# Optimization experiments

Measured on AMD Instinct MI355X. Metric: run time of the kernel, lower is better.

## Reference

```python
import jax, jax.numpy as jnp
import numpy as np

D_MODEL, D_STATE, D_CONV, EXPAND = 1024, 16, 4, 2
D_INNER = D_MODEL * EXPAND
BATCH, SEQ = 2, 2048


def setup_inputs() -> dict:
    key = jax.random.key(0)
    ks = jax.random.split(key, 10)
    s = lambda *sh: 1.0 / np.sqrt(sh[-1])
    x = jax.random.normal(ks[0], (BATCH, SEQ, D_MODEL), jnp.float32)
    W_in = jax.random.normal(ks[1], (2 * D_INNER, D_MODEL), jnp.float32) * s(D_MODEL)
    conv_w = jax.random.normal(ks[2], (D_INNER, 1, D_CONV), jnp.float32) * s(D_CONV)
    conv_b = jax.random.normal(ks[3], (D_INNER,), jnp.float32) * 0.01
    W_x = jax.random.normal(ks[4], (2 * D_STATE + 1, D_INNER), jnp.float32) * s(D_INNER)
    W_dt = jax.random.normal(ks[5], (D_INNER, 1), jnp.float32)
    b_dt = jax.random.normal(ks[6], (D_INNER,), jnp.float32) * 0.01
    A_log = jnp.log(jnp.broadcast_to(jnp.arange(1, D_STATE + 1, dtype=jnp.float32), (D_INNER, D_STATE)))
    D = jnp.ones((D_INNER,), jnp.float32)
    W_out = jax.random.normal(ks[7], (D_MODEL, D_INNER), jnp.float32) * s(D_INNER)
    return {"x": x, "W_in": W_in, "conv_w": conv_w, "conv_b": conv_b,
            "W_x": W_x, "W_dt": W_dt, "b_dt": b_dt, "A_log": A_log, "D": D, "W_out": W_out}


def _selective_ssm(x, W_in, conv_w, conv_b, W_x, W_dt, b_dt, A_log, D, W_out):
    B_, L, _ = x.shape
    d_inner = conv_w.shape[0]
    d_conv = conv_w.shape[-1]
    d_state = A_log.shape[-1]
    # input projection -> (x, z), each [B, L, d_inner]
    xz = jnp.einsum('bld,ed->ble', x, W_in)
    xi, z = jnp.split(xz, 2, axis=-1)
    # depthwise causal conv over time (torch pads both sides then slices [:L] == left-pad)
    x_ncl = jnp.moveaxis(xi, 1, 2)  # [B, d_inner, L]
    x_conv = jax.lax.conv_general_dilated(
        x_ncl, conv_w, window_strides=(1,), padding=[(d_conv - 1, 0)],
        dimension_numbers=('NCH', 'OIH', 'NCH'), feature_group_count=d_inner)
    x_conv = x_conv + conv_b[None, :, None]
    xi = jax.nn.silu(jnp.moveaxis(x_conv, 1, 2))  # [B, L, d_inner]
    # selective parameters
    x_dbl = jnp.einsum('bld,ed->ble', xi, W_x)  # [B, L, 2*d_state+1]
    dt_raw = x_dbl[..., :1]
    Bmat = x_dbl[..., 1:1 + d_state]
    Cmat = x_dbl[..., 1 + d_state:]
    dt = jax.nn.softplus(dt_raw * W_dt[None, None, :, 0] + b_dt)  # [B, L, d_inner]
    A = -jnp.exp(A_log)  # [d_inner, d_state]
    # recurrence: h_t = exp(dt_t*A)*h_{t-1} + (dt_t*B_t)*x_t ; y_t = <h_t, C_t>
    def step(h, inp):
        x_t, dt_t, B_t, C_t = inp  # [B,d], [B,d], [B,n], [B,n]
        dA = jnp.exp(dt_t[..., None] * A)              # [B, d, n]
        dB = dt_t[..., None] * B_t[:, None, :]          # [B, d, n]
        h = dA * h + dB * x_t[..., None]
        y = jnp.einsum('bdn,bn->bd', h, C_t)
        return h, y

    h0 = jnp.zeros((B_, d_inner, d_state), xi.dtype)
    xs = (jnp.moveaxis(xi, 0, 1), jnp.moveaxis(dt, 0, 1),
          jnp.moveaxis(Bmat, 0, 1), jnp.moveaxis(Cmat, 0, 1))
    _, ys = jax.lax.scan(step, h0, xs)                 # [L, B, d_inner]
    y = jnp.moveaxis(ys, 0, 1) + D * xi                # skip term D*x_t
    y = y * jax.nn.silu(z)
    return jnp.einsum('bld,ed->ble', y, W_out)


def reference(x, W_in, conv_w, conv_b, W_x, W_dt, b_dt, A_log, D, W_out):
    return _selective_ssm(x, W_in, conv_w, conv_b, W_x, W_dt, b_dt, A_log, D, W_out)
```

## Files before the change

### kernel.cpp

```cpp
#include <hip/hip_runtime.h>
#include <hip/hip_bf16.h>

#define D_MODEL 1024
#define D_STATE 16
#define D_CONV  4
#define D_INNER 2048
#define BATCH   2
#define SEQ     2048
#define NTOK    (BATCH * SEQ)
#define NXZ     (2 * D_INNER)
#define NDBL    (2 * D_STATE + 1)
#define XROW    40
#define CHUNK   32
#define NCHUNK  (SEQ / CHUNK)
#define XT      4

typedef __attribute__((ext_vector_type(8))) short bf16x8;
typedef __attribute__((ext_vector_type(4))) float f32x4;

__device__ __forceinline__ float silu_fast(float x) {
    return x / (1.0f + __expf(-x));
}
__device__ __forceinline__ float softplus_fast(float x) {
    float r = __logf(1.0f + __expf(x));
    return (x > 20.f) ? x : r;
}
__device__ __forceinline__ short f2bf(float f) {
    __hip_bfloat16 h = __float2bfloat16(f);
    return __builtin_bit_cast(short, h);
}
__device__ __forceinline__ float bf2f(short s) {
    return __bfloat162float(__builtin_bit_cast(__hip_bfloat16, s));
}
__device__ __forceinline__ void gload_lds16(const void* g, void* l) {
    __builtin_amdgcn_global_load_lds(
        (const __attribute__((address_space(1))) void*)g,
        (__attribute__((address_space(3))) void*)l, 16, 0, 0);
}

__global__ void split_kernel(const float* __restrict__ in, short* __restrict__ hi,
                             short* __restrict__ lo, int n4)
{
    int i = blockIdx.x * blockDim.x + threadIdx.x;
    if (i >= n4) return;
    float4 v = ((const float4*)in)[i];
    short4 h, l;
    h.x = f2bf(v.x); l.x = f2bf(v.x - bf2f(h.x));
    h.y = f2bf(v.y); l.y = f2bf(v.y - bf2f(h.y));
    h.z = f2bf(v.z); l.z = f2bf(v.z - bf2f(h.z));
    h.w = f2bf(v.w); l.w = f2bf(v.w - bf2f(h.w));
    ((short4*)hi)[i] = h;
    ((short4*)lo)[i] = l;
}

__launch_bounds__(256, 3)
__global__ void mfma_gemm_split(const short* __restrict__ Ahi, const short* __restrict__ Alo,
                                const short* __restrict__ Bhi, const short* __restrict__ Blo,
                                float* __restrict__ C, int M, int N, int K)
{
    __shared__ short sAh[4096], sAl[4096], sBh[4096], sBl[4096];
    const int tid  = threadIdx.x;
    const int lane = tid & 63;
    const int wave = tid >> 6;
    const int bm = blockIdx.y, bn = blockIdx.x;
    const int wm = wave >> 1, wn = wave & 1;

    const int r0a = bm * 128, r0b = bn * 128;

    auto stage = [&](int k0) {
#pragma unroll
        for (int i = 0; i < 2; ++i) {
            const int off = i * 4096 + tid * 16;
            const int g   = off >> 11;
            const int row = (off >> 4) & 127;
            const size_t ea = (size_t)(r0a + row) * K + k0 + g * 8;
            const size_t eb = (size_t)(r0b + row) * K + k0 + g * 8;
            gload_lds16(Ahi + ea, (char*)sAh + i * 4096 + wave * 1024);
            gload_lds16(Alo + ea, (char*)sAl + i * 4096 + wave * 1024);
            gload_lds16(Bhi + eb, (char*)sBh + i * 4096 + wave * 1024);
            gload_lds16(Blo + eb, (char*)sBl + i * 4096 + wave * 1024);
        }
    };

    f32x4 acc[4][4] = {};

    stage(0);
    for (int k0 = 0; k0 < K; k0 += 32) {
        __syncthreads();

        const int g = lane >> 4;
        bf16x8 ah[4], al[4], bh[4], bl[4];
#pragma unroll
        for (int m = 0; m < 4; ++m) {
            const int rowA = wm * 64 + m * 16 + (lane & 15);
            const int rowB = wn * 64 + m * 16 + (lane & 15);
            ah[m] = ((const bf16x8*)sAh)[g * 128 + rowA];
            al[m] = ((const bf16x8*)sAl)[g * 128 + rowA];
            bh[m] = ((const bf16x8*)sBh)[g * 128 + rowB];
            bl[m] = ((const bf16x8*)sBl)[g * 128 + rowB];
        }
        __syncthreads();

        if (k0 + 32 < K) stage(k0 + 32);

#pragma unroll
        for (int m = 0; m < 4; ++m)
#pragma unroll
            for (int n = 0; n < 4; ++n) {
                acc[m][n] = __builtin_amdgcn_mfma_f32_16x16x32_bf16(ah[m], bh[n], acc[m][n], 0, 0, 0);
                acc[m][n] = __builtin_amdgcn_mfma_f32_16x16x32_bf16(ah[m], bl[n], acc[m][n], 0, 0, 0);
                acc[m][n] = __builtin_amdgcn_mfma_f32_16x16x32_bf16(al[m], bh[n], acc[m][n], 0, 0, 0);
            }
    }

#pragma unroll
    for (int m = 0; m < 4; ++m) {
        const int row = bm * 128 + wm * 64 + m * 16 + ((lane >> 4) << 2);
#pragma unroll
        for (int n = 0; n < 4; ++n) {
            const int col = bn * 128 + wn * 64 + n * 16 + (lane & 15);
#pragma unroll
            for (int r = 0; r < 4; ++r)
                C[(size_t)(row + r) * N + col] = acc[m][n][r];
        }
    }
}

__global__ void conv_silu_kernel(const float* __restrict__ xz,
                                 const float* __restrict__ conv_w,
                                 const float* __restrict__ conv_b,
                                 float* __restrict__ xi)
{
    int idx = blockIdx.x * blockDim.x + threadIdx.x;
    if (idx >= NTOK * D_INNER) return;
    int d = idx % D_INNER;
    int t = idx / D_INNER;
    int l = t % SEQ;
    int b = t / SEQ;

    float w0 = conv_w[d * 4 + 0], w1 = conv_w[d * 4 + 1];
    float w2 = conv_w[d * 4 + 2], w3 = conv_w[d * 4 + 3];

    const float* base = xz + ((size_t)b * SEQ) * NXZ + d;
    float acc = conv_b[d];
    if (l >= 3) acc = fmaf(w0, base[(size_t)(l - 3) * NXZ], acc);
    if (l >= 2) acc = fmaf(w1, base[(size_t)(l - 2) * NXZ], acc);
    if (l >= 1) acc = fmaf(w2, base[(size_t)(l - 1) * NXZ], acc);
    acc = fmaf(w3, base[(size_t)l * NXZ], acc);
    xi[idx] = silu_fast(acc);
}

__launch_bounds__(256)
__global__ void xdbl_kernel(const float* __restrict__ xi,
                            const float* __restrict__ W_x,
                            float* __restrict__ xdbl)
{
    __shared__ float rows[XT][D_INNER];
    const int t0 = blockIdx.x * XT;
    for (int i = threadIdx.x; i < XT * D_INNER; i += 256)
        rows[i >> 11][i & 2047] = xi[(size_t)(t0 + (i >> 11)) * D_INNER + (i & 2047)];
    __syncthreads();

    const int wave = threadIdx.x >> 6;
    const int lane = threadIdx.x & 63;
    for (int e = wave; e < NDBL; e += 4) {
        const float* wr = W_x + (size_t)e * D_INNER;
        float s0 = 0.f, s1 = 0.f, s2 = 0.f, s3 = 0.f;
        for (int i = lane; i < D_INNER; i += 64) {
            float w = wr[i];
            s0 = fmaf(rows[0][i], w, s0);
            s1 = fmaf(rows[1][i], w, s1);
            s2 = fmaf(rows[2][i], w, s2);
            s3 = fmaf(rows[3][i], w, s3);
        }
#pragma unroll
        for (int off = 32; off; off >>= 1) {
            s0 += __shfl_xor(s0, off);
            s1 += __shfl_xor(s1, off);
            s2 += __shfl_xor(s2, off);
            s3 += __shfl_xor(s3, off);
        }
        if (lane == 0) {
            const int slot = (e == 0 ? 0 : e + 3);
            xdbl[(size_t)(t0 + 0) * XROW + slot] = s0;
            xdbl[(size_t)(t0 + 1) * XROW + slot] = s1;
            xdbl[(size_t)(t0 + 2) * XROW + slot] = s2;
            xdbl[(size_t)(t0 + 3) * XROW + slot] = s3;
        }
    }
}

__launch_bounds__(256)
__global__ void scan_pass1(const float* __restrict__ xdbl,
                           const float* __restrict__ xi,
                           const float* __restrict__ W_dt,
                           const float* __restrict__ b_dt,
                           const float* __restrict__ A_log,
                           float* __restrict__ aprod,
                           float* __restrict__ hloc)
{
    const int d = blockIdx.x * 256 + threadIdx.x;
    const int c = blockIdx.y;
    const int b = blockIdx.z;

    float A[16];
    {
        const float4* ar = (const float4*)(A_log + (size_t)d * 16);
#pragma unroll
        for (int q = 0; q < 4; ++q) {
            float4 v = ar[q];
            A[q * 4 + 0] = -__expf(v.x);
            A[q * 4 + 1] = -__expf(v.y);
            A[q * 4 + 2] = -__expf(v.z);
            A[q * 4 + 3] = -__expf(v.w);
        }
    }
    const float wdt = W_dt[d], bdt = b_dt[d];

    const float* xd = xdbl + ((size_t)b * SEQ + c * CHUNK) * XROW;
    const float* xp = xi + ((size_t)b * SEQ + c * CHUNK) * D_INNER + d;

    float h[16], ap[16], Bv[16];
#pragma unroll
    for (int n = 0; n < 16; ++n) { h[n] = 0.f; ap[n] = 1.f; }

    for (int l = 0; l < CHUNK; ++l) {
        float raw = xd[0];
#pragma unroll
        for (int q = 0; q < 4; ++q) {
            float4 v = *(const float4*)(xd + 4 + q * 4);
            Bv[q * 4 + 0] = v.x; Bv[q * 4 + 1] = v.y;
            Bv[q * 4 + 2] = v.z; Bv[q * 4 + 3] = v.w;
        }
        float xv = xp[0];
        float dtv = softplus_fast(fmaf(raw, wdt, bdt));
        float dtx = dtv * xv;
#pragma unroll
        for (int n = 0; n < 16; ++n) {
            float e = __expf(dtv * A[n]);
            h[n]  = fmaf(e, h[n], Bv[n] * dtx);
            ap[n] *= e;
        }
        xd += XROW; xp += D_INNER;
    }

    size_t s = (((size_t)b * NCHUNK + c) * D_INNER + d) * 16;
#pragma unroll
    for (int q = 0; q < 4; ++q) {
        *(float4*)(aprod + s + q * 4) = make_float4(ap[q*4], ap[q*4+1], ap[q*4+2], ap[q*4+3]);
        *(float4*)(hloc  + s + q * 4) = make_float4(h[q*4],  h[q*4+1],  h[q*4+2],  h[q*4+3]);
    }
}

__global__ void scan_combine(float* __restrict__ aprod,
                             const float* __restrict__ hloc)
{
    int idx = blockIdx.x * blockDim.x + threadIdx.x;
    int b  = idx >> 15;
    int dn = idx & 32767;
    float hs = 0.f;
#pragma unroll
    for (int c = 0; c < NCHUNK; ++c) {
        size_t s = (((size_t)b * NCHUNK + c) << 15) + dn;
        float ap = aprod[s];
        float hl = hloc[s];
        aprod[s] = hs;
        hs = fmaf(ap, hs, hl);
    }
}

__launch_bounds__(256)
__global__ void scan_pass2(const float* __restrict__ xdbl,
                           float* __restrict__ xi,
                           const float* __restrict__ xz,
                           const float* __restrict__ W_dt,
                           const float* __restrict__ b_dt,
                           const float* __restrict__ A_log,
                           const float* __restrict__ Dvec,
                           const float* __restrict__ hstart)
{
    const int d = blockIdx.x * 256 + threadIdx.x;
    const int c = blockIdx.y;
    const int b = blockIdx.z;

    float A[16];
    {
        const float4* ar = (const float4*)(A_log + (size_t)d * 16);
#pragma unroll
        for (int q = 0; q < 4; ++q) {
            float4 v = ar[q];
            A[q * 4 + 0] = -__expf(v.x);
            A[q * 4 + 1] = -__expf(v.y);
            A[q * 4 + 2] = -__expf(v.z);
            A[q * 4 + 3] = -__expf(v.w);
        }
    }
    const float wdt = W_dt[d], bdt = b_dt[d], Dd = Dvec[d];

    const float* xd = xdbl + ((size_t)b * SEQ + c * CHUNK) * XROW;
    float*       xp = xi + ((size_t)b * SEQ + c * CHUNK) * D_INNER + d;
    const float* zp = xz + ((size_t)b * SEQ + c * CHUNK) * NXZ + D_INNER + d;

    float h[16], Bv[16], Cv[16];
    {
        size_t s = (((size_t)b * NCHUNK + c) * D_INNER + d) * 16;
#pragma unroll
        for (int q = 0; q < 4; ++q) {
            float4 v = *(const float4*)(hstart + s + q * 4);
            h[q * 4 + 0] = v.x; h[q * 4 + 1] = v.y;
            h[q * 4 + 2] = v.z; h[q * 4 + 3] = v.w;
        }
    }

    for (int l = 0; l < CHUNK; ++l) {
        float raw = xd[0];
#pragma unroll
        for (int q = 0; q < 4; ++q) {
            float4 v = *(const float4*)(xd + 4 + q * 4);
            Bv[q * 4 + 0] = v.x; Bv[q * 4 + 1] = v.y;
            Bv[q * 4 + 2] = v.z; Bv[q * 4 + 3] = v.w;
            float4 w = *(const float4*)(xd + 20 + q * 4);
            Cv[q * 4 + 0] = w.x; Cv[q * 4 + 1] = w.y;
            Cv[q * 4 + 2] = w.z; Cv[q * 4 + 3] = w.w;
        }
        float xv = xp[0];
        float zv = zp[0];
        float dtv = softplus_fast(fmaf(raw, wdt, bdt));
        float dtx = dtv * xv;

        float p0 = 0.f, p1 = 0.f, p2 = 0.f, p3 = 0.f;
#pragma unroll
        for (int q = 0; q < 4; ++q) {
            float e0 = __expf(dtv * A[q*4+0]);
            float e1 = __expf(dtv * A[q*4+1]);
            float e2 = __expf(dtv * A[q*4+2]);
            float e3 = __expf(dtv * A[q*4+3]);
            h[q*4+0] = fmaf(e0, h[q*4+0], Bv[q*4+0] * dtx);
            h[q*4+1] = fmaf(e1, h[q*4+1], Bv[q*4+1] * dtx);
            h[q*4+2] = fmaf(e2, h[q*4+2], Bv[q*4+2] * dtx);
            h[q*4+3] = fmaf(e3, h[q*4+3], Bv[q*4+3] * dtx);
            p0 = fmaf(h[q*4+0], Cv[q*4+0], p0);
            p1 = fmaf(h[q*4+1], Cv[q*4+1], p1);
            p2 = fmaf(h[q*4+2], Cv[q*4+2], p2);
            p3 = fmaf(h[q*4+3], Cv[q*4+3], p3);
        }
        float y = (p0 + p1) + (p2 + p3) + Dd * xv;
        xp[0] = y * silu_fast(zv);

        xd += XROW; xp += D_INNER; zp += NXZ;
    }
}

extern "C" void kernel_launch(void* const* d_in, const int* in_sizes, int n_in,
                              void* d_out, int out_size, void* d_ws, size_t ws_size,
                              hipStream_t stream)
{
    (void)in_sizes; (void)n_in; (void)out_size; (void)ws_size;

    const float* x      = (const float*)d_in[0];
    const float* W_in   = (const float*)d_in[1];
    const float* conv_w = (const float*)d_in[2];
    const float* conv_b = (const float*)d_in[3];
    const float* W_x    = (const float*)d_in[4];
    const float* W_dt   = (const float*)d_in[5];
    const float* b_dt   = (const float*)d_in[6];
    const float* A_log  = (const float*)d_in[7];
    const float* Dvec   = (const float*)d_in[8];
    const float* W_out  = (const float*)d_in[9];
    float* out = (float*)d_out;

    float* xz   = (float*)d_ws;
    float* xi   = xz + (size_t)NTOK * NXZ;
    float* xdbl = xi + (size_t)NTOK * D_INNER;
    float* R    = xdbl + (size_t)NTOK * XROW;

    short* x_hi   = (short*)R;
    short* x_lo   = x_hi + (size_t)NTOK * D_MODEL;
    short* Win_hi = x_lo + (size_t)NTOK * D_MODEL;
    short* Win_lo = Win_hi + (size_t)NXZ * D_MODEL;
    float* aprod  = R;
    float* hloc   = aprod + (size_t)BATCH * NCHUNK * D_INNER * 16;
    short* y_hi   = (short*)xz;
    short* y_lo   = y_hi + (size_t)NTOK * D_INNER;
    short* Wou_hi = y_lo + (size_t)NTOK * D_INNER;
    short* Wou_lo = Wou_hi + (size_t)D_MODEL * D_INNER;

    split_kernel<<<(NTOK * D_MODEL / 4 + 255) / 256, 256, 0, stream>>>(x, x_hi, x_lo, NTOK * D_MODEL / 4);
    split_kernel<<<(NXZ * D_MODEL / 4 + 255) / 256, 256, 0, stream>>>(W_in, Win_hi, Win_lo, NXZ * D_MODEL / 4);

    {
        dim3 grid(NXZ / 128, NTOK / 128);
        mfma_gemm_split<<<grid, 256, 0, stream>>>(x_hi, x_lo, Win_hi, Win_lo, xz, NTOK, NXZ, D_MODEL);
    }
    {
        int total = NTOK * D_INNER;
        conv_silu_kernel<<<(total + 255) / 256, 256, 0, stream>>>(xz, conv_w, conv_b, xi);
    }
    xdbl_kernel<<<NTOK / XT, 256, 0, stream>>>(xi, W_x, xdbl);

    {
        dim3 grid(D_INNER / 256, NCHUNK, BATCH);
        scan_pass1<<<grid, 256, 0, stream>>>(xdbl, xi, W_dt, b_dt, A_log, aprod, hloc);
        scan_combine<<<(BATCH * D_INNER * 16) / 256, 256, 0, stream>>>(aprod, hloc);
        scan_pass2<<<grid, 256, 0, stream>>>(xdbl, xi, xz, W_dt, b_dt, A_log, Dvec, aprod);
    }
    split_kernel<<<(NTOK * D_INNER / 4 + 255) / 256, 256, 0, stream>>>(xi, y_hi, y_lo, NTOK * D_INNER / 4);
    split_kernel<<<(D_MODEL * D_INNER / 4 + 255) / 256, 256, 0, stream>>>(W_out, Wou_hi, Wou_lo, D_MODEL * D_INNER / 4);
    {
        dim3 grid(D_MODEL / 128, NTOK / 128);
        mfma_gemm_split<<<grid, 256, 0, stream>>>(y_hi, y_lo, Wou_hi, Wou_lo, out, NTOK, D_MODEL, D_INNER);
    }
}
```

Measured before the change: 595.7 us.

## Double-buffer LDS in split GEMM, add split-K and XCD-aware block remap

The split-bf16 MFMA GEMM now uses two LDS buffers, so the next K-tile load is issued before computing the current one and one barrier per step is dropped. Workgroup IDs are remapped in groups of 8, apparently to spread adjacent tiles across XCDs. The output projection becomes a 2-way split-K, writing partial results into the free xi buffer, followed by an add kernel. This trades double the LDS (lower occupancy bound) and extra partial-sum traffic for better latency hiding and more workgroups on the small-N GEMM.

```diff
diff --git a/kernel.cpp b/kernel.cpp
--- a/kernel.cpp
+++ b/kernel.cpp
@@ -53,21 +53,33 @@
     ((short4*)lo)[i] = l;
 }
 
-__launch_bounds__(256, 3)
+__launch_bounds__(256, 2)
 __global__ void mfma_gemm_split(const short* __restrict__ Ahi, const short* __restrict__ Alo,
                                 const short* __restrict__ Bhi, const short* __restrict__ Blo,
-                                float* __restrict__ C, int M, int N, int K)
-{
-    __shared__ short sAh[4096], sAl[4096], sBh[4096], sBl[4096];
+                                float* __restrict__ C, int M, int N, int K,
+                                int kLen, size_t partStride)
+{
+    __shared__ short sAh[2][4096], sAl[2][4096], sBh[2][4096], sBl[2][4096];
     const int tid  = threadIdx.x;
     const int lane = tid & 63;
     const int wave = tid >> 6;
-    const int bm = blockIdx.y, bn = blockIdx.x;
     const int wm = wave >> 1, wn = wave & 1;
 
+    const int gx = gridDim.x, gy = gridDim.y;
+    const int nwg = gx * gy * gridDim.z;
+    int f = (blockIdx.z * gy + blockIdx.y) * gx + blockIdx.x;
+    f = (f & 7) * (nwg >> 3) + (f >> 3);
+    const int bz  = f / (gx * gy);
+    const int rem = f % (gx * gy);
+    const int bm = rem / gx;
+    const int bn = rem % gx;
+
+    const int kBeg = bz * kLen;
+    float* Cp = C + (size_t)bz * partStride;
+
     const int r0a = bm * 128, r0b = bn * 128;
 
-    auto stage = [&](int k0) {
+    auto stage = [&](int k0, int buf) {
 #pragma unroll
         for (int i = 0; i < 2; ++i) {
             const int off = i * 4096 + tid * 16;
@@ -75,34 +87,39 @@
             const int row = (off >> 4) & 127;
             const size_t ea = (size_t)(r0a + row) * K + k0 + g * 8;
             const size_t eb = (size_t)(r0b + row) * K + k0 + g * 8;
-            gload_lds16(Ahi + ea, (char*)sAh + i * 4096 + wave * 1024);
-            gload_lds16(Alo + ea, (char*)sAl + i * 4096 + wave * 1024);
-            gload_lds16(Bhi + eb, (char*)sBh + i * 4096 + wave * 1024);
-            gload_lds16(Blo + eb, (char*)sBl + i * 4096 + wave * 1024);
+            const int dst = buf * 8192 + i * 4096 + wave * 1024;
+            gload_lds16(Ahi + ea, (char*)sAh + dst);
+            gload_lds16(Alo + ea, (char*)sAl + dst);
+            gload_lds16(Bhi + eb, (char*)sBh + dst);
+            gload_lds16(Blo + eb, (char*)sBl + dst);
         }
     };
 
     f32x4 acc[4][4] = {};
-
-    stage(0);
-    for (int k0 = 0; k0 < K; k0 += 32) {
+    const int nsteps = kLen / 32;
+
+    stage(kBeg, 0);
+    for (int s = 0; s < nsteps; ++s) {
         __syncthreads();
-
+        if (s + 1 < nsteps) stage(kBeg + (s + 1) * 32, (s + 1) & 1);
+
+        const int buf = s & 1;
         const int g = lane >> 4;
+        const bf16x8* pAh = (const bf16x8*)sAh + buf * 512 + g * 128;
+        const bf16x8* pAl = (const bf16x8*)sAl + buf * 512 + g * 128;
+        const bf16x8* pBh = (const bf16x8*)sBh + buf * 512 + g * 128;
+        const bf16x8* pBl = (const bf16x8*)sBl + buf * 512 + g * 128;
+
         bf16x8 ah[4], al[4], bh[4], bl[4];
 #pragma unroll
         for (int m = 0; m < 4; ++m) {
             const int rowA = wm * 64 + m * 16 + (lane & 15);
             const int rowB = wn * 64 + m * 16 + (lane & 15);
-            ah[m] = ((const bf16x8*)sAh)[g * 128 + rowA];
-            al[m] = ((const bf16x8*)sAl)[g * 128 + rowA];
-            bh[m] = ((const bf16x8*)sBh)[g * 128 + rowB];
-            bl[m] = ((const bf16x8*)sBl)[g * 128 + rowB];
-        }
-        __syncthreads();
-
-        if (k0 + 32 < K) stage(k0 + 32);
-
+            ah[m] = pAh[rowA];
+            al[m] = pAl[rowA];
+            bh[m] = pBh[rowB];
+            bl[m] = pBl[rowB];
+        }
 #pragma unroll
         for (int m = 0; m < 4; ++m)
 #pragma unroll
@@ -121,9 +138,19 @@
             const int col = bn * 128 + wn * 64 + n * 16 + (lane & 15);
 #pragma unroll
             for (int r = 0; r < 4; ++r)
-                C[(size_t)(row + r) * N + col] = acc[m][n][r];
-        }
-    }
+                Cp[(size_t)(row + r) * N + col] = acc[m][n][r];
+        }
+    }
+}
+
+__global__ void add2_kernel(const float* __restrict__ a, const float* __restrict__ b,
+                            float* __restrict__ o, int n4)
+{
+    int i = blockIdx.x * blockDim.x + threadIdx.x;
+    if (i >= n4) return;
+    float4 va = ((const float4*)a)[i];
+    float4 vb = ((const float4*)b)[i];
+    ((float4*)o)[i] = make_float4(va.x + vb.x, va.y + vb.y, va.z + vb.z, va.w + vb.w);
 }
 
 __global__ void conv_silu_kernel(const float* __restrict__ xz,
@@ -384,13 +411,16 @@
     short* y_lo   = y_hi + (size_t)NTOK * D_INNER;
     short* Wou_hi = y_lo + (size_t)NTOK * D_INNER;
     short* Wou_lo = Wou_hi + (size_t)D_MODEL * D_INNER;
+    float* part0  = xi;
+    float* part1  = part0 + (size_t)NTOK * D_MODEL;
 
     split_kernel<<<(NTOK * D_MODEL / 4 + 255) / 256, 256, 0, stream>>>(x, x_hi, x_lo, NTOK * D_MODEL / 4);
     split_kernel<<<(NXZ * D_MODEL / 4 + 255) / 256, 256, 0, stream>>>(W_in, Win_hi, Win_lo, NXZ * D_MODEL / 4);
 
     {
-        dim3 grid(NXZ / 128, NTOK / 128);
-        mfma_gemm_split<<<grid, 256, 0, stream>>>(x_hi, x_lo, Win_hi, Win_lo, xz, NTOK, NXZ, D_MODEL);
+        dim3 grid(NXZ / 128, NTOK / 128, 1);
+        mfma_gemm_split<<<grid, 256, 0, stream>>>(x_hi, x_lo, Win_hi, Win_lo, xz,
+                                                  NTOK, NXZ, D_MODEL, D_MODEL, 0);
     }
     {
         int total = NTOK * D_INNER;
@@ -407,7 +437,10 @@
     split_kernel<<<(NTOK * D_INNER / 4 + 255) / 256, 256, 0, stream>>>(xi, y_hi, y_lo, NTOK * D_INNER / 4);
     split_kernel<<<(D_MODEL * D_INNER / 4 + 255) / 256, 256, 0, stream>>>(W_out, Wou_hi, Wou_lo, D_MODEL * D_INNER / 4);
     {
-        dim3 grid(D_MODEL / 128, NTOK / 128);
-        mfma_gemm_split<<<grid, 256, 0, stream>>>(y_hi, y_lo, Wou_hi, Wou_lo, out, NTOK, D_MODEL, D_INNER);
-    }
-}
+        dim3 grid(D_MODEL / 128, NTOK / 128, 2);
+        mfma_gemm_split<<<grid, 256, 0, stream>>>(y_hi, y_lo, Wou_hi, Wou_lo, part0,
+                                                  NTOK, D_MODEL, D_INNER, D_INNER / 2,
+                                                  (size_t)NTOK * D_MODEL);
+        add2_kernel<<<(NTOK * D_MODEL / 4 + 255) / 256, 256, 0, stream>>>(part0, part1, out, NTOK * D_MODEL / 4);
+    }
+}
```

Result: no change. 599.4 us (+0.6%).
